# Kernel tuning notes

Measured on AMD Instinct MI355X. Metric: run time of the kernel, lower is better.

The kernel has to match this reference:

```python
import jax, jax.numpy as jnp
import numpy as np

N = 100000      # total nodes
G = 500         # graphs
NPG = 200       # nodes per graph
E = 1_600_000   # edges
XS = 128        # input feature dim
FIX = 10        # fixed_size one-hot id dim
H = 64          # hidden (neuron)
NPERM = 3
YS = 1


def setup_inputs() -> dict:
    key = jax.random.key(0)
    ks = jax.random.split(key, 10)
    x = jax.random.normal(ks[0], (N, XS), jnp.float32)

    rng = np.random.default_rng(0)
    src = rng.integers(0, N, E)
    off = rng.integers(1, NPG, E)
    dst = (src // NPG) * NPG + (src % NPG + off) % NPG  # edges stay within graph
    edge_index = jnp.asarray(np.stack([src, dst]).astype(np.int32))
    batch_ids = jnp.asarray((np.arange(N) // NPG).astype(np.int32))

    # permuted tiled-eye node ids: node at local pos p gets one_hot(perm[p] % 10)
    base = np.arange(NPG) % FIX  # tiled eye row indices for one graph
    ids = rng.permuted(np.tile(base, (NPERM, G, 1)), axis=-1).reshape(NPERM, N)
    perm_ids = jax.nn.one_hot(jnp.asarray(ids), FIX, dtype=jnp.float32)

    def lin(k, fin, fout):
        return jax.random.normal(k, (fin, fout), jnp.float32) * (1.0 / np.sqrt(fin))

    return {
        "x": x, "edge_index": edge_index, "batch_ids": batch_ids, "perm_ids": perm_ids,
        "w1": lin(ks[1], XS + FIX, H), "b1": jnp.zeros((H,), jnp.float32),
        "w2": lin(ks[2], H, H), "b2": jnp.zeros((H,), jnp.float32),
        "w3": lin(ks[3], H, H), "b3": jnp.zeros((H,), jnp.float32),
        "a1w": lin(ks[4], H, 16), "a1b": jnp.zeros((16,), jnp.float32),
        "a2w": lin(ks[5], 16, YS), "a2b": jnp.zeros((YS,), jnp.float32),
    }


def reference(x, edge_index, batch_ids, perm_ids,
              w1, b1, w2, b2, w3, b3, a1w, a1b, a2w, a2b):
    src, dst = edge_index[0], edge_index[1]
    loop = jnp.arange(N, dtype=src.dtype)
    src_a = jnp.concatenate([src, loop])  # GCNConv adds self-loops
    dst_a = jnp.concatenate([dst, loop])
    deg = jax.ops.segment_sum(jnp.ones_like(dst_a, x.dtype), dst_a, N)
    dinv = jnp.where(deg > 0, deg ** -0.5, 0.0)
    norm = (dinv[src_a] * dinv[dst_a])[:, None]  # [E+N, 1]

    def conv(h, W, b):
        h = h @ W  # transform first (cheaper: H <= in_dim)
        return jax.ops.segment_sum(h[src_a] * norm, dst_a, N) + b

    counts = jnp.maximum(jax.ops.segment_sum(jnp.ones((N,), x.dtype), batch_ids, G), 1.0)

    out = jnp.zeros((G, H), x.dtype)
    for p in range(NPERM):
        h = jnp.concatenate([x, perm_ids[p]], axis=1)  # [N, XS+FIX]
        h = jax.nn.relu(conv(h, w1, b1))
        h = jax.nn.relu(conv(h, w2, b2))
        h = jax.nn.relu(conv(h, w3, b3))
        hg = jax.ops.segment_sum(h, batch_ids, G) / counts[:, None]  # mean pool
        out = out + hg / NPERM

    out = jax.nn.relu(out @ a1w + a1b)
    return out @ a2w + a2b  # [G, YS]
```

## Files before the change

### kernel.cpp

```cpp
#include <hip/hip_runtime.h>

#define NN   100000
#define EE   1600000
#define GG   500
#define NPGc 200
#define HH   64
#define NPERMc 3
#define C1   16384
#define HST  74
#define BSTRIDE 4096

typedef __fp16   h16x2 __attribute__((ext_vector_type(2)));
typedef _Float16 f16x4 __attribute__((ext_vector_type(4)));
typedef _Float16 f16x8 __attribute__((ext_vector_type(8)));
typedef float    f32x4 __attribute__((ext_vector_type(4)));

__device__ __forceinline__ void cvt_hilo(f32x4 a, f32x4 b, f16x8& hi, f16x8& lo) {
    float f[8] = {a[0], a[1], a[2], a[3], b[0], b[1], b[2], b[3]};
#pragma unroll
    for (int j = 0; j < 8; j += 2) {
        h16x2 h = __builtin_amdgcn_cvt_pkrtz(f[j], f[j + 1]);
        h16x2 l = __builtin_amdgcn_cvt_pkrtz(f[j] - (float)h[0], f[j + 1] - (float)h[1]);
        hi[j] = (_Float16)h[0]; hi[j + 1] = (_Float16)h[1];
        lo[j] = (_Float16)l[0]; lo[j + 1] = (_Float16)l[1];
    }
}

__device__ __forceinline__ void cvt_hilo4(const float (&v)[4], f16x4& hv, f16x4& lv) {
#pragma unroll
    for (int i = 0; i < 4; i += 2) {
        h16x2 h = __builtin_amdgcn_cvt_pkrtz(v[i], v[i + 1]);
        h16x2 l = __builtin_amdgcn_cvt_pkrtz(v[i] - (float)h[0], v[i + 1] - (float)h[1]);
        hv[i] = (_Float16)h[0]; hv[i + 1] = (_Float16)h[1];
        lv[i] = (_Float16)l[0]; lv[i + 1] = (_Float16)l[1];
    }
}

#define EB 98
__global__ __launch_bounds__(512) void k_prep(const int* __restrict__ ei, int* __restrict__ gcnt,
                                              unsigned short* __restrict__ gtok,
                                              const float* __restrict__ w1, const float* __restrict__ w2,
                                              const float* __restrict__ w3, _Float16* __restrict__ wf) {
    int t = threadIdx.x;
    if (blockIdx.x >= EB) {
        int tid = (blockIdx.x - EB) * 512 + t;
        int c = tid >> 6, lane = tid & 63;
        int q = lane >> 4, m = lane & 15;
        const float* src; int kstep, ct, term;
        if (c < 32) { kstep = c & 3; ct = (c >> 2) & 3; term = c >> 4; src = w1; }
        else {
            int c2 = c - 32;
            kstep = c2 & 1; ct = (c2 >> 1) & 3; term = (c2 >> 3) & 1;
            src = (c2 >> 4) ? w3 : w2;
        }
        f16x8 v;
#pragma unroll
        for (int j = 0; j < 8; ++j) {
            int k = kstep * 32 + q * 8 + j;
            int n = ct * 16 + m;
            float wv = src[k * 64 + n];
            _Float16 hi = (_Float16)wv;
            float lo = wv - (float)hi;
            v[j] = term ? (_Float16)lo : hi;
        }
        *((f16x8*)(wf + c * 512) + lane) = v;
        return;
    }
    __shared__ unsigned short stag[C1];
    __shared__ int h[512], esc[512], cur[512], gb[512];
    int base = blockIdx.x * C1;
    int nE = min(C1, EE - base);
    h[t] = 0; cur[t] = 0;
    __syncthreads();
    for (int i = t; i < nE; i += 512) atomicAdd(&h[ei[base + i] / NPGc], 1);
    __syncthreads();
    esc[t] = h[t];
    __syncthreads();
    for (int off = 1; off < 512; off <<= 1) {
        int u = (t >= off) ? esc[t - off] : 0;
        __syncthreads();
        esc[t] += u;
        __syncthreads();
    }
    esc[t] -= h[t];
    if (t < GG && h[t] > 0) gb[t] = atomicAdd(&gcnt[t], h[t]);
    __syncthreads();
    for (int i = t; i < nE; i += 512) {
        int s = ei[base + i], d = ei[EE + base + i];
        int g = s / NPGc;
        int ls = s - g * NPGc, ld = d - g * NPGc;
        int pos = esc[g] + atomicAdd(&cur[g], 1);
        stag[pos] = (unsigned short)(ls | (ld << 8));
    }
    __syncthreads();
    int w = t >> 6, lane = t & 63;
    for (int g = w; g < GG; g += 8) {
        int c = h[g]; if (!c) continue;
        int lb = esc[g], off = gb[g];
        int lim = min(c, BSTRIDE - off);
        for (int j = lane; j < lim; j += 64) gtok[(size_t)g * BSTRIDE + off + j] = stag[lb + j];
    }
}

__global__ __launch_bounds__(256) void k_xw(const float* __restrict__ x,
                                            const _Float16* __restrict__ wf,
                                            float* __restrict__ xW) {
    int lane = threadIdx.x & 63, w = threadIdx.x >> 6;
    int rbase = blockIdx.x * 64 + w * 16;
    int m = lane & 15, q = lane >> 4;
    int row = rbase + m;
    int rowc = min(row, NN - 1);
    f16x8 Ah[4], Al[4];
#pragma unroll
    for (int ks = 0; ks < 4; ++ks) {
        const float* ar = x + (size_t)rowc * 128 + ks * 32 + q * 8;
        f32x4 f0 = *(const f32x4*)ar;
        f32x4 f1 = *(const f32x4*)(ar + 4);
        cvt_hilo(f0, f1, Ah[ks], Al[ks]);
    }
#pragma unroll
    for (int ct = 0; ct < 4; ++ct) {
        f32x4 acc = {0.f, 0.f, 0.f, 0.f};
#pragma unroll
        for (int ks = 0; ks < 4; ++ks) {
            f16x8 Bh = *((const f16x8*)(wf + ((0 * 4 + ct) * 4 + ks) * 512) + lane);
            f16x8 Bl = *((const f16x8*)(wf + ((1 * 4 + ct) * 4 + ks) * 512) + lane);
            acc = __builtin_amdgcn_mfma_f32_16x16x32_f16(Ah[ks], Bh, acc, 0, 0, 0);
            acc = __builtin_amdgcn_mfma_f32_16x16x32_f16(Al[ks], Bh, acc, 0, 0, 0);
            acc = __builtin_amdgcn_mfma_f32_16x16x32_f16(Ah[ks], Bl, acc, 0, 0, 0);
        }
#pragma unroll
        for (int i = 0; i < 4; ++i) {
            int r = rbase + q * 4 + i;
            if (r < NN) xW[(size_t)r * 64 + ct * 16 + m] = acc[i];
        }
    }
}

__device__ __forceinline__ f16x8 cvt_a8(uint2 v) {
    f16x8 r;
#pragma unroll
    for (int k = 0; k < 4; ++k) r[k] = (_Float16)(float)((v.x >> (8 * k)) & 255u);
#pragma unroll
    for (int k = 0; k < 4; ++k) r[4 + k] = (_Float16)(float)((v.y >> (8 * k)) & 255u);
    return r;
}

template <bool POOL>
__device__ __forceinline__ void conv_mfma(const _Float16* __restrict__ Tfh,
                                          const _Float16* __restrict__ Tfl,
                                          float* __restrict__ H,
                                          const f16x8 (&Af)[2][7], int w, int m, int q, int nmt,
                                          const float (&dvv)[2][4], const float (&bias)[4],
                                          float (&poolv)[4]) {
    f32x4 acc[2][4];
#pragma unroll
    for (int mi = 0; mi < 2; ++mi)
#pragma unroll
        for (int ct = 0; ct < 4; ++ct) acc[mi][ct] = (f32x4){0.f, 0.f, 0.f, 0.f};
    int lane = m + 16 * q;
    for (int ks = 0; ks < 7; ++ks) {
#pragma unroll
        for (int ct = 0; ct < 4; ++ct) {
            f16x8 Bh = *((const f16x8*)(Tfh + (ks * 4 + ct) * 512) + lane);
            f16x8 Bl = *((const f16x8*)(Tfl + (ks * 4 + ct) * 512) + lane);
            acc[0][ct] = __builtin_amdgcn_mfma_f32_16x16x32_f16(Af[0][ks], Bh, acc[0][ct], 0, 0, 0);
            acc[0][ct] = __builtin_amdgcn_mfma_f32_16x16x32_f16(Af[0][ks], Bl, acc[0][ct], 0, 0, 0);
            if (nmt > 1) {
                acc[1][ct] = __builtin_amdgcn_mfma_f32_16x16x32_f16(Af[1][ks], Bh, acc[1][ct], 0, 0, 0);
                acc[1][ct] = __builtin_amdgcn_mfma_f32_16x16x32_f16(Af[1][ks], Bl, acc[1][ct], 0, 0, 0);
            }
        }
    }
#pragma unroll
    for (int mi = 0; mi < 2; ++mi) {
        if (mi >= nmt) break;
        int rbase = (w + 8 * mi) * 16 + q * 4;
#pragma unroll
        for (int ct = 0; ct < 4; ++ct) {
            if (!POOL) {
#pragma unroll
                for (int i = 0; i < 4; ++i)
                    H[(rbase + i) * HST + ct * 16 + m] =
                        fmaxf(fmaf(dvv[mi][i], acc[mi][ct][i], bias[ct]), 0.f);
            } else {
                float pl = 0.f;
#pragma unroll
                for (int i = 0; i < 4; ++i) {
                    float o = fmaxf(fmaf(dvv[mi][i], acc[mi][ct][i], bias[ct]), 0.f);
                    if (rbase + i < NPGc) pl += o;
                }
                poolv[ct] += pl;
            }
        }
    }
}

__device__ __forceinline__ void gemm_mfma(const float* __restrict__ H,
                                          _Float16* __restrict__ Tfh, _Float16* __restrict__ Tfl,
                                          const _Float16* __restrict__ wf, int w, int lane,
                                          int m, int q, int nmt, const float (&dvv)[2][4]) {
#pragma unroll
    for (int mi = 0; mi < 2; ++mi) {
        if (mi >= nmt) break;
        int mt = w + 8 * mi;
        f16x8 Ah[2], Al[2];
#pragma unroll
        for (int ks = 0; ks < 2; ++ks) {
            const float* ap = H + (mt * 16 + m) * HST + ks * 32 + 8 * q;
            float2 u0 = *(const float2*)ap;
            float2 u1 = *(const float2*)(ap + 2);
            float2 u2 = *(const float2*)(ap + 4);
            float2 u3 = *(const float2*)(ap + 6);
            f32x4 a = {u0.x, u0.y, u1.x, u1.y};
            f32x4 b = {u2.x, u2.y, u3.x, u3.y};
            cvt_hilo(a, b, Ah[ks], Al[ks]);
        }
        int quad = ((mt & 1) << 1) + (q >> 1);
        int j0 = (q & 1) << 2;
        int lanep = m + (quad << 4);
#pragma unroll
        for (int ct = 0; ct < 4; ++ct) {
            f32x4 acc = {0.f, 0.f, 0.f, 0.f};
#pragma unroll
            for (int ks = 0; ks < 2; ++ks) {
                f16x8 Bh = *((const f16x8*)(wf + ((0 * 4 + ct) * 2 + ks) * 512) + lane);
                f16x8 Bl = *((const f16x8*)(wf + ((1 * 4 + ct) * 2 + ks) * 512) + lane);
                acc = __builtin_amdgcn_mfma_f32_16x16x32_f16(Ah[ks], Bh, acc, 0, 0, 0);
                acc = __builtin_amdgcn_mfma_f32_16x16x32_f16(Al[ks], Bh, acc, 0, 0, 0);
                acc = __builtin_amdgcn_mfma_f32_16x16x32_f16(Ah[ks], Bl, acc, 0, 0, 0);
            }
            float o[4];
#pragma unroll
            for (int i = 0; i < 4; ++i) o[i] = acc[i] * dvv[mi][i];
            f16x4 hv, lv;
            cvt_hilo4(o, hv, lv);
            int off = ((mt >> 1) * 4 + ct) * 512 + lanep * 8 + j0;
            *(f16x4*)(Tfh + off) = hv;
            *(f16x4*)(Tfl + off) = lv;
        }
    }
}

__global__ __launch_bounds__(512, 2) void k_fused(
    const float* __restrict__ xW, const float* __restrict__ perm,
    const float* __restrict__ w1tail,
    const float* __restrict__ b1, const float* __restrict__ b2, const float* __restrict__ b3,
    const _Float16* __restrict__ wsW23,
    const int* __restrict__ gcnt, const unsigned short* __restrict__ gtok,
    const float* __restrict__ a1w, const float* __restrict__ a1b,
    const float* __restrict__ a2w, const float* __restrict__ a2b,
    float* __restrict__ out) {
    __shared__ __align__(16) float Hm[15392];
    __shared__ __align__(16) _Float16 Tfh[28 * 512];
    __shared__ __align__(16) _Float16 Tfl[28 * 512];
    __shared__ __align__(16) _Float16 wlds[16384];
    __shared__ float w1r[640];
    __shared__ float dv[224];
    __shared__ float pool[8 * 64];
    __shared__ unsigned char idsl[672];

    unsigned char* A8  = (unsigned char*)Hm;
    unsigned int*  A32 = (unsigned int*)Hm;

    int g = blockIdx.x, t = threadIdx.x;
    int lane = t & 63, w = t >> 6;
    int m = lane & 15, q = lane >> 4;
    int nbase = g * NPGc;
    int cnt = min(gcnt[g], BSTRIDE);
    const unsigned short* tok = gtok + (size_t)g * BSTRIDE;

    for (int i = t; i < 2048; i += 512) ((f16x8*)wlds)[i] = ((const f16x8*)wsW23)[i];
    for (int i = t; i < 640; i += 512) w1r[i] = w1tail[i];
    for (int i = t; i < 2912; i += 512) ((uint4*)A8)[i] = make_uint4(0, 0, 0, 0);
    __syncthreads();
    for (int i = t; i < cnt; i += 512) {
        int tk = tok[i];
        int addr = (tk >> 8) * 224 + (tk & 255);
        atomicAdd(&A32[addr >> 2], 1u << ((addr & 3) * 8));
    }
    if (t < NPGc) { int a = t * 225; atomicAdd(&A32[a >> 2], 1u << ((a & 3) * 8)); }
    for (int i = t; i < 672; i += 512) {
        int p = i / 224, nd = i - p * 224;
        int id = 0;
        if (nd < NPGc) {
            const float* pp = perm + ((size_t)p * NN + nbase + nd) * 10;
            float best = pp[0];
#pragma unroll
            for (int k = 1; k < 10; ++k) { float v = pp[k]; if (v > best) { best = v; id = k; } }
        }
        idsl[i] = (unsigned char)id;
    }
    __syncthreads();
    if (t < 224) {
        unsigned s = 0;
        if (t < 208)
            for (int i = 0; i < 56; ++i) {
                unsigned v = A32[t * 56 + i];
                s += (v & 255u) + ((v >> 8) & 255u) + ((v >> 16) & 255u) + (v >> 24);
            }
        dv[t] = s ? rsqrtf((float)s) : 0.f;
    }
    int nmt = (w < 5) ? 2 : 1;
    f16x8 Af[2][7];
#pragma unroll
    for (int mi = 0; mi < 2; ++mi) {
        int mt = w + 8 * mi;
        if (mt < 13) {
#pragma unroll
            for (int ks = 0; ks < 7; ++ks) {
                uint2 v = *(const uint2*)(A8 + (mt * 16 + m) * 224 + ks * 32 + q * 8);
                Af[mi][ks] = cvt_a8(v);
            }
        }
    }
    __syncthreads();

    float dvv[2][4];
#pragma unroll
    for (int mi = 0; mi < 2; ++mi)
#pragma unroll
        for (int i = 0; i < 4; ++i) {
            int r = (w + 8 * mi) * 16 + q * 4 + i;
            dvv[mi][i] = (w + 8 * mi < 13) ? dv[r] : 0.f;
        }
    float bb1[4], bb2[4], bb3[4];
#pragma unroll
    for (int ct = 0; ct < 4; ++ct) {
        bb1[ct] = b1[ct * 16 + m]; bb2[ct] = b2[ct * 16 + m]; bb3[ct] = b3[ct * 16 + m];
    }

    float poolv[4] = {0.f, 0.f, 0.f, 0.f};

    for (int p = 0; p < NPERMc; ++p) {
        {
            const unsigned char* ids = idsl + p * 224;
            for (int nd0 = w * 28; nd0 < w * 28 + 28; nd0 += 4) {
                float vals[4];
#pragma unroll
                for (int i = 0; i < 4; ++i) {
                    int nd = nd0 + i;
                    float v = 0.f;
                    if (nd < NPGc) {
                        int id = ids[nd];
                        v = dv[nd] * (xW[(size_t)(nbase + nd) * 64 + lane] + w1r[id * 64 + lane]);
                    }
                    vals[i] = v;
                }
                f16x4 hv, lv;
                cvt_hilo4(vals, hv, lv);
                int c = (nd0 >> 5) * 4 + (lane >> 4);
                int lanep = (lane & 15) + (((nd0 & 31) >> 3) << 4);
                int off = c * 512 + lanep * 8 + (nd0 & 7);
                *(f16x4*)(Tfh + off) = hv;
                *(f16x4*)(Tfl + off) = lv;
            }
        }
        __syncthreads();
        conv_mfma<false>(Tfh, Tfl, Hm, Af, w, m, q, nmt, dvv, bb1, poolv);
        __syncthreads();
        gemm_mfma(Hm, Tfh, Tfl, wlds, w, lane, m, q, nmt, dvv);
        __syncthreads();
        conv_mfma<false>(Tfh, Tfl, Hm, Af, w, m, q, nmt, dvv, bb2, poolv);
        __syncthreads();
        gemm_mfma(Hm, Tfh, Tfl, wlds + 8192, w, lane, m, q, nmt, dvv);
        __syncthreads();
        conv_mfma<true>(Tfh, Tfl, Hm, Af, w, m, q, nmt, dvv, bb3, poolv);
        __syncthreads();
    }

#pragma unroll
    for (int ct = 0; ct < 4; ++ct) {
        float v = poolv[ct];
        v += __shfl_xor(v, 16);
        v += __shfl_xor(v, 32);
        if (q == 0) pool[w * 64 + ct * 16 + m] = v;
    }
    __syncthreads();
    if (t < 64) {
        float tot = 0.f;
#pragma unroll
        for (int i = 0; i < 8; ++i) tot += pool[i * 64 + t];
        pool[t] = tot * (1.0f / (NPGc * NPERMc));
    }
    __syncthreads();
    if (t < 16) {
        float a = a1b[t];
        for (int k = 0; k < 64; ++k) a = fmaf(pool[k], a1w[k * 16 + t], a);
        pool[64 + t] = fmaxf(a, 0.f);
    }
    __syncthreads();
    if (t == 0) {
        float o = a2b[0];
#pragma unroll
        for (int i = 0; i < 16; ++i) o = fmaf(pool[64 + i], a2w[i], o);
        out[g] = o;
    }
}


static inline size_t alignup(size_t x) { return (x + 255) & ~(size_t)255; }

extern "C" void kernel_launch(void* const* d_in, const int* in_sizes, int n_in,
                              void* d_out, int out_size, void* d_ws, size_t ws_size,
                              hipStream_t stream) {
    const float* x    = (const float*)d_in[0];
    const int*   ei   = (const int*)d_in[1];
    const float* perm = (const float*)d_in[3];
    const float* w1   = (const float*)d_in[4];
    const float* b1   = (const float*)d_in[5];
    const float* w2   = (const float*)d_in[6];
    const float* b2   = (const float*)d_in[7];
    const float* w3   = (const float*)d_in[8];
    const float* b3   = (const float*)d_in[9];
    const float* a1w  = (const float*)d_in[10];
    const float* a1b  = (const float*)d_in[11];
    const float* a2w  = (const float*)d_in[12];
    const float* a2b  = (const float*)d_in[13];
    float* out = (float*)d_out;

    char* p = (char*)d_ws;
    auto take = [&](size_t bytes) { char* r = p; p += alignup(bytes); return r; };
    float*          xW   = (float*)take((size_t)NN * 64 * 4);
    unsigned short* gtok = (unsigned short*)take((size_t)GG * BSTRIDE * 2);
    _Float16*       wsW  = (_Float16*)take((size_t)64 * 512 * 2);
    int*            gcnt = (int*)take(512 * 4);
    (void)hipMemsetAsync(gcnt, 0, 512 * 4, stream);

    k_prep<<<EB + 8, 512, 0, stream>>>(ei, gcnt, gtok, w1, w2, w3, wsW);
    k_xw<<<(NN + 63) / 64, 256, 0, stream>>>(x, wsW, xW);
    k_fused<<<GG, 512, 0, stream>>>(xW, perm, w1 + 128 * 64, b1, b2, b3,
                                    wsW + 32 * 512, gcnt, gtok,
                                    a1w, a1b, a2w, a2b, out);
}
```

Baseline: 277.4 us.

## Build dense per-graph adjacency globally and drop fp16 hi/lo split in convs

Replaces the edge bucketing prep kernel with a direct global-atomic kernel that builds a dense 8-bit adjacency matrix per graph, preceded by a large memset. The fused kernel now reads its adjacency fragments straight from global memory and computes degrees with shuffles. In the conv and hidden GEMM stages it drops the fp16 hi/lo error-compensation terms, using single fp16 operands and storing activations as fp16, which halves the MFMA and LDS traffic. The k_xw kernel now stages x and the w1 fragments in LDS with larger blocks. Taken together this trades numerical accuracy for less compute and raises occupancy (launch bounds 4).

New measurement: 319.1 us. 1.15x slower.

```diff
diff --git a/kernel.cpp b/kernel.cpp
--- a/kernel.cpp
+++ b/kernel.cpp
@@ -4,11 +4,8 @@
 #define EE   1600000
 #define GG   500
 #define NPGc 200
-#define HH   64
 #define NPERMc 3
-#define C1   16384
-#define HST  74
-#define BSTRIDE 4096
+#define ASTRIDE (208 * 224)
 
 typedef __fp16   h16x2 __attribute__((ext_vector_type(2)));
 typedef _Float16 f16x4 __attribute__((ext_vector_type(4)));
@@ -26,169 +23,153 @@
     }
 }
 
-__device__ __forceinline__ void cvt_hilo4(const float (&v)[4], f16x4& hv, f16x4& lv) {
-#pragma unroll
-    for (int i = 0; i < 4; i += 2) {
-        h16x2 h = __builtin_amdgcn_cvt_pkrtz(v[i], v[i + 1]);
-        h16x2 l = __builtin_amdgcn_cvt_pkrtz(v[i] - (float)h[0], v[i + 1] - (float)h[1]);
-        hv[i] = (_Float16)h[0]; hv[i + 1] = (_Float16)h[1];
-        lv[i] = (_Float16)l[0]; lv[i + 1] = (_Float16)l[1];
-    }
-}
-
-#define EB 98
-__global__ __launch_bounds__(512) void k_prep(const int* __restrict__ ei, int* __restrict__ gcnt,
-                                              unsigned short* __restrict__ gtok,
-                                              const float* __restrict__ w1, const float* __restrict__ w2,
-                                              const float* __restrict__ w3, _Float16* __restrict__ wf) {
-    int t = threadIdx.x;
-    if (blockIdx.x >= EB) {
-        int tid = (blockIdx.x - EB) * 512 + t;
-        int c = tid >> 6, lane = tid & 63;
-        int q = lane >> 4, m = lane & 15;
-        const float* src; int kstep, ct, term;
-        if (c < 32) { kstep = c & 3; ct = (c >> 2) & 3; term = c >> 4; src = w1; }
-        else {
-            int c2 = c - 32;
-            kstep = c2 & 1; ct = (c2 >> 1) & 3; term = (c2 >> 3) & 1;
-            src = (c2 >> 4) ? w3 : w2;
-        }
-        f16x8 v;
-#pragma unroll
-        for (int j = 0; j < 8; ++j) {
-            int k = kstep * 32 + q * 8 + j;
-            int n = ct * 16 + m;
-            float wv = src[k * 64 + n];
-            _Float16 hi = (_Float16)wv;
-            float lo = wv - (float)hi;
-            v[j] = term ? (_Float16)lo : hi;
-        }
-        *((f16x8*)(wf + c * 512) + lane) = v;
-        return;
-    }
-    __shared__ unsigned short stag[C1];
-    __shared__ int h[512], esc[512], cur[512], gb[512];
-    int base = blockIdx.x * C1;
-    int nE = min(C1, EE - base);
-    h[t] = 0; cur[t] = 0;
-    __syncthreads();
-    for (int i = t; i < nE; i += 512) atomicAdd(&h[ei[base + i] / NPGc], 1);
-    __syncthreads();
-    esc[t] = h[t];
-    __syncthreads();
-    for (int off = 1; off < 512; off <<= 1) {
-        int u = (t >= off) ? esc[t - off] : 0;
-        __syncthreads();
-        esc[t] += u;
-        __syncthreads();
-    }
-    esc[t] -= h[t];
-    if (t < GG && h[t] > 0) gb[t] = atomicAdd(&gcnt[t], h[t]);
-    __syncthreads();
-    for (int i = t; i < nE; i += 512) {
-        int s = ei[base + i], d = ei[EE + base + i];
+__device__ __forceinline__ f16x4 cvt4h(const float (&v)[4]) {
+    f16x4 r;
+    h16x2 a = __builtin_amdgcn_cvt_pkrtz(v[0], v[1]);
+    h16x2 b = __builtin_amdgcn_cvt_pkrtz(v[2], v[3]);
+    r[0] = (_Float16)a[0]; r[1] = (_Float16)a[1];
+    r[2] = (_Float16)b[0]; r[3] = (_Float16)b[1];
+    return r;
+}
+
+__device__ __forceinline__ f16x8 wfrag_slot(const float* __restrict__ src, int kstep, int ct,
+                                            int term, int mq, int qq) {
+    f16x8 v;
+#pragma unroll
+    for (int j = 0; j < 8; ++j) {
+        float wv = src[(kstep * 32 + qq * 8 + j) * 64 + ct * 16 + mq];
+        _Float16 hi = (_Float16)wv;
+        v[j] = term ? (_Float16)(wv - (float)hi) : hi;
+    }
+    return v;
+}
+
+__device__ __forceinline__ f16x8 cvt_a8(uint2 v) {
+    f16x8 r;
+#pragma unroll
+    for (int k = 0; k < 4; ++k) r[k] = (_Float16)(float)((v.x >> (8 * k)) & 255u);
+#pragma unroll
+    for (int k = 0; k < 4; ++k) r[4 + k] = (_Float16)(float)((v.y >> (8 * k)) & 255u);
+    return r;
+}
+
+__global__ __launch_bounds__(256) void k_adj(const int* __restrict__ ei, unsigned int* __restrict__ A) {
+    int idx = blockIdx.x * 256 + threadIdx.x;
+    if (idx < EE) {
+        int s = ei[idx], d = ei[EE + idx];
         int g = s / NPGc;
         int ls = s - g * NPGc, ld = d - g * NPGc;
-        int pos = esc[g] + atomicAdd(&cur[g], 1);
-        stag[pos] = (unsigned short)(ls | (ld << 8));
-    }
-    __syncthreads();
-    int w = t >> 6, lane = t & 63;
-    for (int g = w; g < GG; g += 8) {
-        int c = h[g]; if (!c) continue;
-        int lb = esc[g], off = gb[g];
-        int lim = min(c, BSTRIDE - off);
-        for (int j = lane; j < lim; j += 64) gtok[(size_t)g * BSTRIDE + off + j] = stag[lb + j];
-    }
-}
-
-__global__ __launch_bounds__(256) void k_xw(const float* __restrict__ x,
-                                            const _Float16* __restrict__ wf,
+        int addr = g * ASTRIDE + ld * 224 + ls;
+        atomicAdd(&A[addr >> 2], 1u << ((addr & 3) * 8));
+    } else if (idx < EE + NN) {
+        int n = idx - EE;
+        int g = n / NPGc, ln = n - g * NPGc;
+        int addr = g * ASTRIDE + ln * 225;
+        atomicAdd(&A[addr >> 2], 1u << ((addr & 3) * 8));
+    }
+}
+
+__global__ __launch_bounds__(512) void k_xw(const float* __restrict__ x,
+                                            const float* __restrict__ w1,
                                             float* __restrict__ xW) {
-    int lane = threadIdx.x & 63, w = threadIdx.x >> 6;
-    int rbase = blockIdx.x * 64 + w * 16;
+    __shared__ __align__(16) float xs[128 * 132];
+    __shared__ __align__(16) _Float16 wf1[32 * 512];
+
+    int t = threadIdx.x;
+    int rbase = blockIdx.x * 128;
+
+    for (int i = t; i < 2048; i += 512) {
+        int c = i >> 6, lane2 = i & 63;
+        ((f16x8*)wf1)[i] = wfrag_slot(w1, c & 3, (c >> 2) & 3, c >> 4, lane2 & 15, lane2 >> 4);
+    }
+    {
+        int row = t >> 5, col4 = t & 31;
+#pragma unroll
+        for (int pass = 0; pass < 8; ++pass) {
+            int r = pass * 16 + row;
+            int grow = min(rbase + r, NN - 1);
+            *(f32x4*)&xs[r * 132 + col4 * 4] = *(const f32x4*)(x + (size_t)grow * 128 + col4 * 4);
+        }
+    }
+    __syncthreads();
+
+    int lane = t & 63, w = t >> 6;
     int m = lane & 15, q = lane >> 4;
-    int row = rbase + m;
-    int rowc = min(row, NN - 1);
+    int rowl = w * 16 + m;
     f16x8 Ah[4], Al[4];
 #pragma unroll
     for (int ks = 0; ks < 4; ++ks) {
-        const float* ar = x + (size_t)rowc * 128 + ks * 32 + q * 8;
-        f32x4 f0 = *(const f32x4*)ar;
-        f32x4 f1 = *(const f32x4*)(ar + 4);
+        f32x4 f0 = *(const f32x4*)&xs[rowl * 132 + ks * 32 + q * 8];
+        f32x4 f1 = *(const f32x4*)&xs[rowl * 132 + ks * 32 + q * 8 + 4];
         cvt_hilo(f0, f1, Ah[ks], Al[ks]);
     }
+    int rb = rbase + w * 16;
 #pragma unroll
     for (int ct = 0; ct < 4; ++ct) {
         f32x4 acc = {0.f, 0.f, 0.f, 0.f};
 #pragma unroll
         for (int ks = 0; ks < 4; ++ks) {
-            f16x8 Bh = *((const f16x8*)(wf + ((0 * 4 + ct) * 4 + ks) * 512) + lane);
-            f16x8 Bl = *((const f16x8*)(wf + ((1 * 4 + ct) * 4 + ks) * 512) + lane);
+            f16x8 Bh = ((const f16x8*)wf1)[((0 * 4 + ct) * 4 + ks) * 64 + lane];
+            f16x8 Bl = ((const f16x8*)wf1)[((1 * 4 + ct) * 4 + ks) * 64 + lane];
             acc = __builtin_amdgcn_mfma_f32_16x16x32_f16(Ah[ks], Bh, acc, 0, 0, 0);
             acc = __builtin_amdgcn_mfma_f32_16x16x32_f16(Al[ks], Bh, acc, 0, 0, 0);
             acc = __builtin_amdgcn_mfma_f32_16x16x32_f16(Ah[ks], Bl, acc, 0, 0, 0);
         }
 #pragma unroll
         for (int i = 0; i < 4; ++i) {
-            int r = rbase + q * 4 + i;
+            int r = rb + q * 4 + i;
             if (r < NN) xW[(size_t)r * 64 + ct * 16 + m] = acc[i];
         }
     }
-}
-
-__device__ __forceinline__ f16x8 cvt_a8(uint2 v) {
-    f16x8 r;
-#pragma unroll
-    for (int k = 0; k < 4; ++k) r[k] = (_Float16)(float)((v.x >> (8 * k)) & 255u);
-#pragma unroll
-    for (int k = 0; k < 4; ++k) r[4 + k] = (_Float16)(float)((v.y >> (8 * k)) & 255u);
-    return r;
 }
 
 template <bool POOL>
 __device__ __forceinline__ void conv_mfma(const _Float16* __restrict__ Tfh,
-                                          const _Float16* __restrict__ Tfl,
-                                          float* __restrict__ H,
-                                          const f16x8 (&Af)[2][7], int w, int m, int q, int nmt,
-                                          const float (&dvv)[2][4], const float (&bias)[4],
+                                          _Float16* __restrict__ Hf,
+                                          const f16x8 (&Af)[2][7], int lane, int m, int q,
+                                          int w, int nmt, const float* __restrict__ dv,
+                                          const float* __restrict__ biasrow,
                                           float (&poolv)[4]) {
     f32x4 acc[2][4];
 #pragma unroll
     for (int mi = 0; mi < 2; ++mi)
 #pragma unroll
         for (int ct = 0; ct < 4; ++ct) acc[mi][ct] = (f32x4){0.f, 0.f, 0.f, 0.f};
-    int lane = m + 16 * q;
+
+#pragma unroll
     for (int ks = 0; ks < 7; ++ks) {
 #pragma unroll
         for (int ct = 0; ct < 4; ++ct) {
-            f16x8 Bh = *((const f16x8*)(Tfh + (ks * 4 + ct) * 512) + lane);
-            f16x8 Bl = *((const f16x8*)(Tfl + (ks * 4 + ct) * 512) + lane);
+            f16x8 Bh = ((const f16x8*)Tfh)[(ks * 4 + ct) * 64 + lane];
             acc[0][ct] = __builtin_amdgcn_mfma_f32_16x16x32_f16(Af[0][ks], Bh, acc[0][ct], 0, 0, 0);
-            acc[0][ct] = __builtin_amdgcn_mfma_f32_16x16x32_f16(Af[0][ks], Bl, acc[0][ct], 0, 0, 0);
-            if (nmt > 1) {
+            if (nmt > 1)
                 acc[1][ct] = __builtin_amdgcn_mfma_f32_16x16x32_f16(Af[1][ks], Bh, acc[1][ct], 0, 0, 0);
-                acc[1][ct] = __builtin_amdgcn_mfma_f32_16x16x32_f16(Af[1][ks], Bl, acc[1][ct], 0, 0, 0);
-            }
         }
     }
 #pragma unroll
     for (int mi = 0; mi < 2; ++mi) {
         if (mi >= nmt) break;
-        int rbase = (w + 8 * mi) * 16 + q * 4;
+        int mt = w + 8 * mi;
+        int rb = mt * 16 + q * 4;
+        float dvi[4];
+#pragma unroll
+        for (int i = 0; i < 4; ++i) dvi[i] = dv[rb + i];
 #pragma unroll
         for (int ct = 0; ct < 4; ++ct) {
+            float bias = biasrow[ct * 16 + m];
             if (!POOL) {
 #pragma unroll
-                for (int i = 0; i < 4; ++i)
-                    H[(rbase + i) * HST + ct * 16 + m] =
-                        fmaxf(fmaf(dvv[mi][i], acc[mi][ct][i], bias[ct]), 0.f);
+                for (int i = 0; i < 4; ++i) {
+                    float o = fmaxf(fmaf(dvi[i], acc[mi][ct][i], bias), 0.f);
+                    Hf[(mt * 2 + (ct >> 1)) * 512 +
+                       ((q * 4 + i) + 16 * ((ct & 1) * 2 + (m >> 3))) * 8 + (m & 7)] = (_Float16)o;
+                }
             } else {
                 float pl = 0.f;
 #pragma unroll
                 for (int i = 0; i < 4; ++i) {
-                    float o = fmaxf(fmaf(dvv[mi][i], acc[mi][ct][i], bias[ct]), 0.f);
-                    if (rbase + i < NPGc) pl += o;
+                    float o = fmaxf(fmaf(dvi[i], acc[mi][ct][i], bias), 0.f);
+                    if (rb + i < NPGc) pl += o;
                 }
                 poolv[ct] += pl;
             }
@@ -196,90 +177,70 @@
     }
 }
 
-__device__ __forceinline__ void gemm_mfma(const float* __restrict__ H,
-                                          _Float16* __restrict__ Tfh, _Float16* __restrict__ Tfl,
-                                          const _Float16* __restrict__ wf, int w, int lane,
-                                          int m, int q, int nmt, const float (&dvv)[2][4]) {
+__device__ __forceinline__ void gemm_mfma(const _Float16* __restrict__ Hf,
+                                          _Float16* __restrict__ Tfh,
+                                          const _Float16* __restrict__ wf, int lane,
+                                          int m, int q, int w, int nmt,
+                                          const float* __restrict__ dv) {
 #pragma unroll
     for (int mi = 0; mi < 2; ++mi) {
         if (mi >= nmt) break;
         int mt = w + 8 * mi;
-        f16x8 Ah[2], Al[2];
-#pragma unroll
-        for (int ks = 0; ks < 2; ++ks) {
-            const float* ap = H + (mt * 16 + m) * HST + ks * 32 + 8 * q;
-            float2 u0 = *(const float2*)ap;
-            float2 u1 = *(const float2*)(ap + 2);
-            float2 u2 = *(const float2*)(ap + 4);
-            float2 u3 = *(const float2*)(ap + 6);
-            f32x4 a = {u0.x, u0.y, u1.x, u1.y};
-            f32x4 b = {u2.x, u2.y, u3.x, u3.y};
-            cvt_hilo(a, b, Ah[ks], Al[ks]);
-        }
-        int quad = ((mt & 1) << 1) + (q >> 1);
+        f16x8 Ah0 = ((const f16x8*)Hf)[(mt * 2 + 0) * 64 + lane];
+        f16x8 Ah1 = ((const f16x8*)Hf)[(mt * 2 + 1) * 64 + lane];
+        float dvi[4];
+#pragma unroll
+        for (int i = 0; i < 4; ++i) dvi[i] = dv[mt * 16 + q * 4 + i];
+        int quad = (2 * mt + (q >> 1)) & 3;
         int j0 = (q & 1) << 2;
         int lanep = m + (quad << 4);
 #pragma unroll
         for (int ct = 0; ct < 4; ++ct) {
             f32x4 acc = {0.f, 0.f, 0.f, 0.f};
-#pragma unroll
-            for (int ks = 0; ks < 2; ++ks) {
-                f16x8 Bh = *((const f16x8*)(wf + ((0 * 4 + ct) * 2 + ks) * 512) + lane);
-                f16x8 Bl = *((const f16x8*)(wf + ((1 * 4 + ct) * 2 + ks) * 512) + lane);
-                acc = __builtin_amdgcn_mfma_f32_16x16x32_f16(Ah[ks], Bh, acc, 0, 0, 0);
-                acc = __builtin_amdgcn_mfma_f32_16x16x32_f16(Al[ks], Bh, acc, 0, 0, 0);
-                acc = __builtin_amdgcn_mfma_f32_16x16x32_f16(Ah[ks], Bl, acc, 0, 0, 0);
-            }
+            f16x8 B0 = ((const f16x8*)wf)[(ct * 2 + 0) * 64 + lane];
+            f16x8 B1 = ((const f16x8*)wf)[(ct * 2 + 1) * 64 + lane];
+            acc = __builtin_amdgcn_mfma_f32_16x16x32_f16(Ah0, B0, acc, 0, 0, 0);
+            acc = __builtin_amdgcn_mfma_f32_16x16x32_f16(Ah1, B1, acc, 0, 0, 0);
             float o[4];
 #pragma unroll
-            for (int i = 0; i < 4; ++i) o[i] = acc[i] * dvv[mi][i];
-            f16x4 hv, lv;
-            cvt_hilo4(o, hv, lv);
-            int off = ((mt >> 1) * 4 + ct) * 512 + lanep * 8 + j0;
-            *(f16x4*)(Tfh + off) = hv;
-            *(f16x4*)(Tfl + off) = lv;
-        }
-    }
-}
-
-__global__ __launch_bounds__(512, 2) void k_fused(
+            for (int i = 0; i < 4; ++i) o[i] = acc[i] * dvi[i];
+            *(f16x4*)(Tfh + ((mt >> 1) * 4 + ct) * 512 + lanep * 8 + j0) = cvt4h(o);
+        }
+    }
+}
+
+__global__ __launch_bounds__(512, 4) void k_fused(
     const float* __restrict__ xW, const float* __restrict__ perm,
-    const float* __restrict__ w1tail,
+    const float* __restrict__ w1,
     const float* __restrict__ b1, const float* __restrict__ b2, const float* __restrict__ b3,
-    const _Float16* __restrict__ wsW23,
-    const int* __restrict__ gcnt, const unsigned short* __restrict__ gtok,
+    const float* __restrict__ w2, const float* __restrict__ w3,
+    const unsigned char* __restrict__ Aall,
     const float* __restrict__ a1w, const float* __restrict__ a1b,
     const float* __restrict__ a2w, const float* __restrict__ a2b,
     float* __restrict__ out) {
-    __shared__ __align__(16) float Hm[15392];
     __shared__ __align__(16) _Float16 Tfh[28 * 512];
-    __shared__ __align__(16) _Float16 Tfl[28 * 512];
-    __shared__ __align__(16) _Float16 wlds[16384];
+    __shared__ __align__(16) _Float16 Hf[26 * 512];
+    __shared__ __align__(16) _Float16 wlds[16 * 512];
     __shared__ float w1r[640];
     __shared__ float dv[224];
+    __shared__ float biasL[192];
     __shared__ float pool[8 * 64];
     __shared__ unsigned char idsl[672];
-
-    unsigned char* A8  = (unsigned char*)Hm;
-    unsigned int*  A32 = (unsigned int*)Hm;
 
     int g = blockIdx.x, t = threadIdx.x;
     int lane = t & 63, w = t >> 6;
     int m = lane & 15, q = lane >> 4;
+    int nmt = (w < 5) ? 2 : 1;
     int nbase = g * NPGc;
-    int cnt = min(gcnt[g], BSTRIDE);
-    const unsigned short* tok = gtok + (size_t)g * BSTRIDE;
-
-    for (int i = t; i < 2048; i += 512) ((f16x8*)wlds)[i] = ((const f16x8*)wsW23)[i];
-    for (int i = t; i < 640; i += 512) w1r[i] = w1tail[i];
-    for (int i = t; i < 2912; i += 512) ((uint4*)A8)[i] = make_uint4(0, 0, 0, 0);
-    __syncthreads();
-    for (int i = t; i < cnt; i += 512) {
-        int tk = tok[i];
-        int addr = (tk >> 8) * 224 + (tk & 255);
-        atomicAdd(&A32[addr >> 2], 1u << ((addr & 3) * 8));
-    }
-    if (t < NPGc) { int a = t * 225; atomicAdd(&A32[a >> 2], 1u << ((a & 3) * 8)); }
+
+    for (int i = t; i < 1024; i += 512) {
+        int c = i >> 6, lane2 = i & 63;
+        const float* src = (c >= 8) ? w3 : w2;
+        int c4 = c & 7;
+        ((f16x8*)wlds)[i] = wfrag_slot(src, c4 & 1, c4 >> 1, 0, lane2 & 15, lane2 >> 4);
+    }
+    for (int i = t; i < 640; i += 512) w1r[i] = w1[128 * 64 + i];
+    if (t < 192) biasL[t] = (t < 64) ? b1[t] : ((t < 128) ? b2[t - 64] : b3[t - 128]);
     for (int i = t; i < 672; i += 512) {
         int p = i / 224, nd = i - p * 224;
         int id = 0;
@@ -291,44 +252,26 @@
         }
         idsl[i] = (unsigned char)id;
     }
-    __syncthreads();
-    if (t < 224) {
+    const unsigned char* Ag = Aall + (size_t)g * ASTRIDE;
+    f16x8 Af[2][7];
+#pragma unroll
+    for (int mi = 0; mi < 2; ++mi) {
+        if (mi >= nmt) break;
+        int mt = w + 8 * mi;
         unsigned s = 0;
-        if (t < 208)
-            for (int i = 0; i < 56; ++i) {
-                unsigned v = A32[t * 56 + i];
-                s += (v & 255u) + ((v >> 8) & 255u) + ((v >> 16) & 255u) + (v >> 24);
-            }
-        dv[t] = s ? rsqrtf((float)s) : 0.f;
-    }
-    int nmt = (w < 5) ? 2 : 1;
-    f16x8 Af[2][7];
-#pragma unroll
-    for (int mi = 0; mi < 2; ++mi) {
-        int mt = w + 8 * mi;
-        if (mt < 13) {
-#pragma unroll
-            for (int ks = 0; ks < 7; ++ks) {
-                uint2 v = *(const uint2*)(A8 + (mt * 16 + m) * 224 + ks * 32 + q * 8);
-                Af[mi][ks] = cvt_a8(v);
-            }
-        }
-    }
-    __syncthreads();
-
-    float dvv[2][4];
-#pragma unroll
-    for (int mi = 0; mi < 2; ++mi)
-#pragma unroll
-        for (int i = 0; i < 4; ++i) {
-            int r = (w + 8 * mi) * 16 + q * 4 + i;
-            dvv[mi][i] = (w + 8 * mi < 13) ? dv[r] : 0.f;
-        }
-    float bb1[4], bb2[4], bb3[4];
-#pragma unroll
-    for (int ct = 0; ct < 4; ++ct) {
-        bb1[ct] = b1[ct * 16 + m]; bb2[ct] = b2[ct * 16 + m]; bb3[ct] = b3[ct * 16 + m];
-    }
+#pragma unroll
+        for (int ks = 0; ks < 7; ++ks) {
+            uint2 v = *(const uint2*)(Ag + (mt * 16 + m) * 224 + ks * 32 + q * 8);
+            Af[mi][ks] = cvt_a8(v);
+            s += (v.x & 255u) + ((v.x >> 8) & 255u) + ((v.x >> 16) & 255u) + (v.x >> 24);
+            s += (v.y & 255u) + ((v.y >> 8) & 255u) + ((v.y >> 16) & 255u) + (v.y >> 24);
+        }
+        float tot = (float)s;
+        tot += __shfl_xor(tot, 16);
+        tot += __shfl_xor(tot, 32);
+        if (q == 0) dv[mt * 16 + m] = (tot > 0.f) ? rsqrtf(tot) : 0.f;
+    }
+    __syncthreads();
 
     float poolv[4] = {0.f, 0.f, 0.f, 0.f};
 
@@ -341,31 +284,25 @@
                 for (int i = 0; i < 4; ++i) {
                     int nd = nd0 + i;
                     float v = 0.f;
-                    if (nd < NPGc) {
-                        int id = ids[nd];
-                        v = dv[nd] * (xW[(size_t)(nbase + nd) * 64 + lane] + w1r[id * 64 + lane]);
-                    }
+                    if (nd < NPGc)
+                        v = dv[nd] * (xW[(size_t)(nbase + nd) * 64 + lane] + w1r[ids[nd] * 64 + lane]);
                     vals[i] = v;
                 }
-                f16x4 hv, lv;
-                cvt_hilo4(vals, hv, lv);
                 int c = (nd0 >> 5) * 4 + (lane >> 4);
                 int lanep = (lane & 15) + (((nd0 & 31) >> 3) << 4);
-                int off = c * 512 + lanep * 8 + (nd0 & 7);
-                *(f16x4*)(Tfh + off) = hv;
-                *(f16x4*)(Tfl + off) = lv;
+                *(f16x4*)(Tfh + c * 512 + lanep * 8 + (nd0 & 7)) = cvt4h(vals);
             }
         }
         __syncthreads();
-        conv_mfma<false>(Tfh, Tfl, Hm, Af, w, m, q, nmt, dvv, bb1, poolv);
-        __syncthreads();
-        gemm_mfma(Hm, Tfh, Tfl, wlds, w, lane, m, q, nmt, dvv);
-        __syncthreads();
-        conv_mfma<false>(Tfh, Tfl, Hm, Af, w, m, q, nmt, dvv, bb2, poolv);
-        __syncthreads();
-        gemm_mfma(Hm, Tfh, Tfl, wlds + 8192, w, lane, m, q, nmt, dvv);
-        __syncthreads();
-        conv_mfma<true>(Tfh, Tfl, Hm, Af, w, m, q, nmt, dvv, bb3, poolv);
+        conv_mfma<false>(Tfh, Hf, Af, lane, m, q, w, nmt, dv, biasL, poolv);
+        __syncthreads();
+        gemm_mfma(Hf, Tfh, wlds, lane, m, q, w, nmt, dv);
+        __syncthreads();
+        conv_mfma<false>(Tfh, Hf, Af, lane, m, q, w, nmt, dv, biasL + 64, poolv);
+        __syncthreads();
+        gemm_mfma(Hf, Tfh, wlds + 8 * 512, lane, m, q, w, nmt, dv);
+        __syncthreads();
+        conv_mfma<true>(Tfh, Hf, Af, lane, m, q, w, nmt, dv, biasL + 128, poolv);
         __syncthreads();
     }
 
@@ -421,15 +358,12 @@
 
     char* p = (char*)d_ws;
     auto take = [&](size_t bytes) { char* r = p; p += alignup(bytes); return r; };
-    float*          xW   = (float*)take((size_t)NN * 64 * 4);
-    unsigned short* gtok = (unsigned short*)take((size_t)GG * BSTRIDE * 2);
-    _Float16*       wsW  = (_Float16*)take((size_t)64 * 512 * 2);
-    int*            gcnt = (int*)take(512 * 4);
-    (void)hipMemsetAsync(gcnt, 0, 512 * 4, stream);
-
-    k_prep<<<EB + 8, 512, 0, stream>>>(ei, gcnt, gtok, w1, w2, w3, wsW);
-    k_xw<<<(NN + 63) / 64, 256, 0, stream>>>(x, wsW, xW);
-    k_fused<<<GG, 512, 0, stream>>>(xW, perm, w1 + 128 * 64, b1, b2, b3,
-                                    wsW + 32 * 512, gcnt, gtok,
+    float*         xW   = (float*)take((size_t)NN * 64 * 4);
+    unsigned char* Aall = (unsigned char*)take((size_t)GG * ASTRIDE);
+    (void)hipMemsetAsync(Aall, 0, (size_t)GG * ASTRIDE, stream);
+
+    k_adj<<<(EE + NN + 255) / 256, 256, 0, stream>>>(ei, (unsigned int*)Aall);
+    k_xw<<<(NN + 127) / 128, 512, 0, stream>>>(x, w1, xW);
+    k_fused<<<GG, 512, 0, stream>>>(xW, perm, w1, b1, b2, b3, w2, w3, Aall,
                                     a1w, a1b, a2w, a2b, out);
 }
```
